# Kernel tuning notes

Measured on AMD Instinct MI355X. Metric: run time of the kernel, lower is better.

## Reference

```python
import jax, jax.numpy as jnp
import numpy as np

N_NODES = 100000
N_EDGES = 600000
HIDDEN = 128


def setup_inputs() -> dict:
    key = jax.random.key(0)
    ks = jax.random.split(key, 5)
    x = jax.random.normal(ks[0], (N_NODES, HIDDEN), dtype=jnp.float32)
    edge_index = jax.random.randint(ks[1], (2, N_EDGES), 0, N_NODES, dtype=jnp.int64)
    edge_weight = jax.random.uniform(ks[2], (N_EDGES,), dtype=jnp.float32)
    # MLP params: Linear(2*H+1 -> H), ReLU, Linear(H -> 1)
    W1 = jax.random.normal(ks[3], (2 * HIDDEN + 1, HIDDEN), dtype=jnp.float32) * (1.0 / np.sqrt(2 * HIDDEN + 1))
    b1 = jnp.zeros((HIDDEN,), dtype=jnp.float32)
    W2 = jax.random.normal(ks[4], (HIDDEN, 1), dtype=jnp.float32) * (1.0 / np.sqrt(HIDDEN))
    b2 = jnp.zeros((1,), dtype=jnp.float32)
    return {"x": x, "edge_index": edge_index, "edge_weight": edge_weight,
            "W1": W1, "b1": b1, "W2": W2, "b2": b2}


def reference(x, edge_index, edge_weight, W1, b1, W2, b2):
    num_nodes = x.shape[0]
    src = edge_index[0]
    tgt = edge_index[1]
    h_src = x[src]                      # [E, H] gather
    h_tgt = x[tgt]                      # [E, H] gather
    w = edge_weight[:, None]            # [E, 1]
    concat = jnp.concatenate([h_src, h_tgt, w], axis=-1)   # [E, 2H+1]
    hidden = jax.nn.relu(concat @ W1 + b1)                 # [E, H]
    scores = (hidden @ W2 + b2)[:, 0]                      # [E]
    # NOTE: the original _softmax_edge's max-pass uses index_put_(accumulate=True)
    # on a -inf buffer, so every touched entry stays -inf and is then replaced by 0;
    # the net effect is NO max subtraction. Faithful math: plain exp / segment_sum.
    exp_scores = jnp.exp(scores)
    sum_exp = jax.ops.segment_sum(exp_scores, tgt, num_segments=num_nodes)
    sum_exp = jnp.maximum(sum_exp, 1e-12)
    alpha = exp_scores / sum_exp[tgt]                      # [E]
    out = jax.ops.segment_sum(alpha[:, None] * h_src, tgt, num_segments=num_nodes)
    return x + out
```

## Files before the change

### kernel.cpp

```cpp
#include <hip/hip_runtime.h>
#include <hip/hip_bf16.h>

#define N_NODES 100000
#define N_EDGES 600000
#define HID 128
#define SCAN_NB ((N_NODES + 255) / 256)


typedef short bf16x8 __attribute__((ext_vector_type(8)));
typedef float f32x4  __attribute__((ext_vector_type(4)));

__device__ inline unsigned short f2bf(float v) {
    __hip_bfloat16 h = __float2bfloat16(v);
    return *(unsigned short*)&h;
}
__device__ inline float bf2f(unsigned short s) {
    unsigned int u = (unsigned int)s << 16;
    return __uint_as_float(u);
}
__device__ inline float2 bfpair(unsigned int u) {
    float lo = __uint_as_float(u << 16);
    float hi = __uint_as_float(u & 0xffff0000u);
    return make_float2(lo, hi);
}

__global__ __launch_bounds__(256) void k_prep(const float* __restrict__ W1,
                                              unsigned short* __restrict__ Bh,
                                              int* __restrict__ deg)
{
    int idx = blockIdx.x * 256 + threadIdx.x;
    if (idx < N_NODES) deg[idx] = 0;
    if (idx < 32768) {
        int n = idx & 255;
        int k = idx >> 8;
        float v = (n < HID) ? W1[k * HID + n] : W1[(HID + k) * HID + (n - HID)];
        int dst = (k >> 5) * 8192 + n * 32 + (k & 31);
        Bh[dst] = f2bf(v);
    }
}

__global__ __launch_bounds__(256) void k_gemm(const float* __restrict__ x,
                                              const unsigned short* __restrict__ BhG,
                                              unsigned short* __restrict__ zbuf,
                                              unsigned short* __restrict__ y2buf)
{
    __shared__ unsigned short Ah[64 * 32];

    const int tid  = threadIdx.x;
    const int bm   = blockIdx.x * 64;
    const int wave = tid >> 6;
    const int lane = tid & 63;
    const int q    = lane >> 4;
    const int ln   = lane & 15;

    const int rowA = tid >> 3;
    const int rowB = rowA + 32;
    const int f4   = tid & 7;
    const int gmA  = bm + rowA;
    const int gmB  = bm + rowB;
    const bool okA = gmA < N_NODES;
    const bool okB = gmB < N_NODES;
    const float* pxA = &x[(size_t)gmA * HID + f4 * 4];
    const float* pxB = &x[(size_t)gmB * HID + f4 * 4];

    f32x4 acc[4][4] = {};

    float4 vA = make_float4(0.f,0.f,0.f,0.f), vB = vA;
    float4 vAn = vA, vBn = vA;
    if (okA) vA = *(const float4*)pxA;
    if (okB) vB = *(const float4*)pxB;

    for (int ks = 0; ks < 4; ++ks) {
        const int k0 = ks * 32;
        {
            float4 v = vA;
            unsigned int ph0 = (unsigned int)f2bf(v.x) | ((unsigned int)f2bf(v.y) << 16);
            unsigned int ph1 = (unsigned int)f2bf(v.z) | ((unsigned int)f2bf(v.w) << 16);
            *(uint2*)&Ah[rowA * 32 + f4 * 4] = make_uint2(ph0, ph1);
            if (okA) *(uint2*)&zbuf[(size_t)gmA * 256 + 128 + k0 + f4 * 4] = make_uint2(ph0, ph1);
        }
        {
            float4 v = vB;
            unsigned int ph0 = (unsigned int)f2bf(v.x) | ((unsigned int)f2bf(v.y) << 16);
            unsigned int ph1 = (unsigned int)f2bf(v.z) | ((unsigned int)f2bf(v.w) << 16);
            *(uint2*)&Ah[rowB * 32 + f4 * 4] = make_uint2(ph0, ph1);
            if (okB) *(uint2*)&zbuf[(size_t)gmB * 256 + 128 + k0 + f4 * 4] = make_uint2(ph0, ph1);
        }
        __syncthreads();

        if (ks < 3) {
            vAn = okA ? *(const float4*)(pxA + (ks + 1) * 32) : make_float4(0.f,0.f,0.f,0.f);
            vBn = okB ? *(const float4*)(pxB + (ks + 1) * 32) : make_float4(0.f,0.f,0.f,0.f);
        }

        bf16x8 ah[4], bh[4];
        #pragma unroll
        for (int mt = 0; mt < 4; ++mt) {
            ah[mt] = *(const bf16x8*)&Ah[(mt * 16 + ln) * 32 + q * 8];
        }
        #pragma unroll
        for (int nt = 0; nt < 4; ++nt) {
            bh[nt] = *(const bf16x8*)&BhG[ks * 8192 + (wave * 64 + nt * 16 + ln) * 32 + q * 8];
        }
        #pragma unroll
        for (int mt = 0; mt < 4; ++mt) {
            #pragma unroll
            for (int nt = 0; nt < 4; ++nt) {
                acc[mt][nt] = __builtin_amdgcn_mfma_f32_16x16x32_bf16(ah[mt], bh[nt], acc[mt][nt], 0, 0, 0);
            }
        }
        __syncthreads();
        vA = vAn; vB = vBn;
    }

    #pragma unroll
    for (int mt = 0; mt < 4; ++mt) {
        #pragma unroll
        for (int r = 0; r < 4; ++r) {
            int row = bm + mt * 16 + q * 4 + r;
            if (row < N_NODES) {
                #pragma unroll
                for (int nt = 0; nt < 4; ++nt) {
                    int col = wave * 64 + nt * 16 + ln;
                    unsigned short v = f2bf(acc[mt][nt][r]);
                    if (col < 128) zbuf[(size_t)row * 256 + col] = v;
                    else           y2buf[(size_t)row * 128 + (col - 128)] = v;
                }
            }
        }
    }
}

__global__ __launch_bounds__(256) void k_count(const int* __restrict__ ei,
                                               int* __restrict__ deg)
{
    int e = blockIdx.x * blockDim.x + threadIdx.x;
    if (e < N_EDGES) atomicAdd(&deg[ei[N_EDGES + e]], 1);
}

__global__ __launch_bounds__(256) void k_partial(const int* __restrict__ deg,
                                                 int* __restrict__ partial)
{
    __shared__ int s[256];
    int t = threadIdx.x;
    int idx = blockIdx.x * 256 + t;
    s[t] = (idx < N_NODES) ? deg[idx] : 0;
    __syncthreads();
    #pragma unroll
    for (int off = 128; off > 0; off >>= 1) {
        if (t < off) s[t] += s[t + off];
        __syncthreads();
    }
    if (t == 0) partial[blockIdx.x] = s[0];
}

__global__ __launch_bounds__(512) void k_scanp(const int* __restrict__ partial,
                                               int* __restrict__ pbase)
{
    __shared__ int s[512];
    int t = threadIdx.x;
    int v = (t < SCAN_NB) ? partial[t] : 0;
    s[t] = v;
    __syncthreads();
    #pragma unroll
    for (int off = 1; off < 512; off <<= 1) {
        int u = (t >= off) ? s[t - off] : 0;
        __syncthreads();
        s[t] += u;
        __syncthreads();
    }
    if (t < SCAN_NB) pbase[t] = s[t] - v;
}

__global__ __launch_bounds__(256) void k_rowptr(const int* __restrict__ deg,
                                                const int* __restrict__ pbase,
                                                int* __restrict__ rowptr,
                                                int* __restrict__ cursor)
{
    __shared__ int s[256];
    int t = threadIdx.x;
    int b = blockIdx.x;
    int idx = b * 256 + t;
    int v = (idx < N_NODES) ? deg[idx] : 0;
    s[t] = v;
    __syncthreads();
    #pragma unroll
    for (int off = 1; off < 256; off <<= 1) {
        int u = (t >= off) ? s[t - off] : 0;
        __syncthreads();
        s[t] += u;
        __syncthreads();
    }
    if (idx < N_NODES) {
        int r = pbase[b] + s[t] - v;
        rowptr[idx] = r;
        cursor[idx] = r;
    }
    if (idx == 0) rowptr[N_NODES] = N_EDGES;
}

__global__ __launch_bounds__(256) void k_fill(const int* __restrict__ ei,
                                              const float* __restrict__ ew,
                                              int* __restrict__ cursor,
                                              uint2* __restrict__ eprs)
{
    int e = blockIdx.x * blockDim.x + threadIdx.x;
    if (e >= N_EDGES) return;
    int tgt = ei[N_EDGES + e];
    int pos = atomicAdd(&cursor[tgt], 1);
    eprs[pos] = make_uint2((unsigned int)ei[e], __float_as_uint(ew[e]));
}

__global__ __launch_bounds__(256) void k_fused(const unsigned int* __restrict__ zu,
                                               const unsigned int* __restrict__ y2u,
                                               const int* __restrict__ rowptr,
                                               const uint2* __restrict__ eprs,
                                               const float* __restrict__ x,
                                               const float* __restrict__ W1,
                                               const float* __restrict__ b1,
                                               const float* __restrict__ W2,
                                               const float* __restrict__ b2,
                                               float* __restrict__ out)
{
    int n = (blockIdx.x * blockDim.x + threadIdx.x) >> 6;
    int lane = threadIdx.x & 63;
    if (n >= N_NODES) return;
    int ql = lane & 15;
    int qi = lane >> 4;
    int c0 = ql * 8;

    uint4 uy2 = *(const uint4*)&y2u[(size_t)n * 64 + ql * 4];
    float2 y2a = bfpair(uy2.x), y2b = bfpair(uy2.y), y2c = bfpair(uy2.z), y2d = bfpair(uy2.w);
    float4 bv0 = *(const float4*)&b1[c0];
    float4 bv1 = *(const float4*)&b1[c0 + 4];
    float4 wr0 = *(const float4*)&W1[256 * HID + c0];
    float4 wr1 = *(const float4*)&W1[256 * HID + c0 + 4];
    float4 w20 = *(const float4*)&W2[c0];
    float4 w21 = *(const float4*)&W2[c0 + 4];
    float p0 = y2a.x + bv0.x, p1 = y2a.y + bv0.y, p2 = y2b.x + bv0.z, p3 = y2b.y + bv0.w;
    float p4 = y2c.x + bv1.x, p5 = y2c.y + bv1.y, p6 = y2d.x + bv1.z, p7 = y2d.y + bv1.w;
    float b2v = b2[0];

    int beg = rowptr[n], end = rowptr[n + 1];
    float a0 = 0.f, a1 = 0.f, a2 = 0.f, a3 = 0.f;
    float a4 = 0.f, a5 = 0.f, a6 = 0.f, a7 = 0.f;
    float denom = 0.f;

    for (int i = beg; i < end; i += 4) {
        int idx = i + qi;
        bool valid = idx < end;
        int ie = valid ? idx : (end - 1);
        uint2 ep = eprs[ie];
        size_t base = (size_t)ep.x * 128;
        float w = __uint_as_float(ep.y);
        uint4 uy = *(const uint4*)&zu[base + ql * 4];
        uint4 ux = *(const uint4*)&zu[base + 64 + ql * 4];

        float2 ya = bfpair(uy.x), yb = bfpair(uy.y), yc = bfpair(uy.z), yd = bfpair(uy.w);
        float h0 = fmaxf(fmaf(w, wr0.x, ya.x + p0), 0.f);
        float h1 = fmaxf(fmaf(w, wr0.y, ya.y + p1), 0.f);
        float h2 = fmaxf(fmaf(w, wr0.z, yb.x + p2), 0.f);
        float h3 = fmaxf(fmaf(w, wr0.w, yb.y + p3), 0.f);
        float h4 = fmaxf(fmaf(w, wr1.x, yc.x + p4), 0.f);
        float h5 = fmaxf(fmaf(w, wr1.y, yc.y + p5), 0.f);
        float h6 = fmaxf(fmaf(w, wr1.z, yd.x + p6), 0.f);
        float h7 = fmaxf(fmaf(w, wr1.w, yd.y + p7), 0.f);
        float s = ((h0 * w20.x + h1 * w20.y) + (h2 * w20.z + h3 * w20.w))
                + ((h4 * w21.x + h5 * w21.y) + (h6 * w21.z + h7 * w21.w));
        #pragma unroll
        for (int m = 1; m <= 8; m <<= 1) s += __shfl_xor(s, m, 64);
        float es = valid ? __expf(s + b2v) : 0.f;

        float2 xa = bfpair(ux.x), xb = bfpair(ux.y), xc = bfpair(ux.z), xd = bfpair(ux.w);
        a0 = fmaf(es, xa.x, a0); a1 = fmaf(es, xa.y, a1);
        a2 = fmaf(es, xb.x, a2); a3 = fmaf(es, xb.y, a3);
        a4 = fmaf(es, xc.x, a4); a5 = fmaf(es, xc.y, a5);
        a6 = fmaf(es, xd.x, a6); a7 = fmaf(es, xd.y, a7);
        denom += es;
    }

    #pragma unroll
    for (int m = 16; m <= 32; m <<= 1) {
        a0 += __shfl_xor(a0, m, 64); a1 += __shfl_xor(a1, m, 64);
        a2 += __shfl_xor(a2, m, 64); a3 += __shfl_xor(a3, m, 64);
        a4 += __shfl_xor(a4, m, 64); a5 += __shfl_xor(a5, m, 64);
        a6 += __shfl_xor(a6, m, 64); a7 += __shfl_xor(a7, m, 64);
        denom += __shfl_xor(denom, m, 64);
    }

    if (qi == 0) {
        float4 xt0 = *(const float4*)&x[(size_t)n * HID + c0];
        float4 xt1 = *(const float4*)&x[(size_t)n * HID + c0 + 4];
        float inv = 1.0f / fmaxf(denom, 1e-12f);
        float4 o0, o1;
        o0.x = xt0.x + a0 * inv; o0.y = xt0.y + a1 * inv;
        o0.z = xt0.z + a2 * inv; o0.w = xt0.w + a3 * inv;
        o1.x = xt1.x + a4 * inv; o1.y = xt1.y + a5 * inv;
        o1.z = xt1.z + a6 * inv; o1.w = xt1.w + a7 * inv;
        *(float4*)&out[(size_t)n * HID + c0]     = o0;
        *(float4*)&out[(size_t)n * HID + c0 + 4] = o1;
    }
}

extern "C" void kernel_launch(void* const* d_in, const int* in_sizes, int n_in,
                              void* d_out, int out_size, void* d_ws, size_t ws_size,
                              hipStream_t stream) {
    const float* x  = (const float*)d_in[0];
    const int*   ei = (const int*)d_in[1];
    const float* ew = (const float*)d_in[2];
    const float* W1 = (const float*)d_in[3];
    const float* b1 = (const float*)d_in[4];
    const float* W2 = (const float*)d_in[5];
    const float* b2 = (const float*)d_in[6];
    float* out = (float*)d_out;
    char* ws = (char*)d_ws;

    const size_t deg_b    = 400000;
    const size_t rowptr_b = 400016;
    const size_t cursor_b = 400000;
    const size_t eprs_b   = 4800000;
    const size_t part_b   = 1568;
    const size_t pb_b     = 1568;
    const size_t Bh_b     = 65536;

    char* p = ws;
    int* deg      = (int*)p;             p += deg_b;
    int* rowptr   = (int*)p;             p += rowptr_b;
    int* cursor   = (int*)p;             p += cursor_b;
    uint2* eprs   = (uint2*)p;           p += eprs_b;
    int* partial  = (int*)p;             p += part_b;
    int* pbase    = (int*)p;             p += pb_b;
    unsigned short* BhG = (unsigned short*)p;  p += Bh_b;
    unsigned short* zbuf  = (unsigned short*)p;  p += (size_t)N_NODES * 256 * 2;
    unsigned short* y2buf = (unsigned short*)p;

    const int edge_blocks = (N_EDGES + 255) / 256;
    const int node_wave_blocks = (N_NODES * 64 + 255) / 256;
    const int gemm_blocks = (N_NODES + 63) / 64;

    hipLaunchKernelGGL(k_prep, dim3(SCAN_NB), dim3(256), 0, stream, W1, BhG, deg);
    hipLaunchKernelGGL(k_count, dim3(edge_blocks), dim3(256), 0, stream, ei, deg);
    hipLaunchKernelGGL(k_partial, dim3(SCAN_NB), dim3(256), 0, stream, deg, partial);
    hipLaunchKernelGGL(k_scanp, dim3(1), dim3(512), 0, stream, partial, pbase);
    hipLaunchKernelGGL(k_rowptr, dim3(SCAN_NB), dim3(256), 0, stream, deg, pbase, rowptr, cursor);
    hipLaunchKernelGGL(k_fill, dim3(edge_blocks), dim3(256), 0, stream, ei, ew, cursor, eprs);
    hipLaunchKernelGGL(k_gemm, dim3(gemm_blocks), dim3(256), 0, stream, x, BhG, zbuf, y2buf);
    hipLaunchKernelGGL(k_fused, dim3(node_wave_blocks), dim3(256), 0, stream,
                       (const unsigned int*)zbuf, (const unsigned int*)y2buf,
                       rowptr, eprs, x, W1, b1, W2, b2, out);
}
```

Baseline: 277.0 us.

## Merge CSR build into cooperative kernel and co-schedule fill with GEMM

```diff
diff --git a/kernel.cpp b/kernel.cpp
--- a/kernel.cpp
+++ b/kernel.cpp
@@ -1,10 +1,15 @@
 #include <hip/hip_runtime.h>
 #include <hip/hip_bf16.h>
+#include <hip/hip_cooperative_groups.h>
+
+namespace cg = cooperative_groups;
 
 #define N_NODES 100000
 #define N_EDGES 600000
 #define HID 128
-#define SCAN_NB ((N_NODES + 255) / 256)
+#define SCAN_NB 391
+#define GEMM_BLOCKS 1563
+#define FILL_BLOCKS 586
 
 
 typedef short bf16x8 __attribute__((ext_vector_type(8)));
@@ -13,10 +18,6 @@
 __device__ inline unsigned short f2bf(float v) {
     __hip_bfloat16 h = __float2bfloat16(v);
     return *(unsigned short*)&h;
-}
-__device__ inline float bf2f(unsigned short s) {
-    unsigned int u = (unsigned int)s << 16;
-    return __uint_as_float(u);
 }
 __device__ inline float2 bfpair(unsigned int u) {
     float lo = __uint_as_float(u << 16);
@@ -24,27 +25,85 @@
     return make_float2(lo, hi);
 }
 
-__global__ __launch_bounds__(256) void k_prep(const float* __restrict__ W1,
-                                              unsigned short* __restrict__ Bh,
-                                              int* __restrict__ deg)
+__global__ __launch_bounds__(256) void k_csr(const float* __restrict__ W1,
+                                             const int* __restrict__ ei,
+                                             unsigned short* __restrict__ Bh,
+                                             int* __restrict__ deg,
+                                             int* __restrict__ partial,
+                                             int* __restrict__ rowptr,
+                                             int* __restrict__ cursor)
 {
-    int idx = blockIdx.x * 256 + threadIdx.x;
-    if (idx < N_NODES) deg[idx] = 0;
-    if (idx < 32768) {
-        int n = idx & 255;
-        int k = idx >> 8;
+    cg::grid_group grid = cg::this_grid();
+    const int tid  = threadIdx.x;
+    const int b    = blockIdx.x;
+    const int gtid = b * 256 + tid;
+
+    if (gtid < N_NODES) deg[gtid] = 0;
+    if (gtid == 0) rowptr[N_NODES] = N_EDGES;
+    if (gtid < 32768) {
+        int n = gtid & 255;
+        int k = gtid >> 8;
         float v = (n < HID) ? W1[k * HID + n] : W1[(HID + k) * HID + (n - HID)];
-        int dst = (k >> 5) * 8192 + n * 32 + (k & 31);
-        Bh[dst] = f2bf(v);
-    }
-}
-
-__global__ __launch_bounds__(256) void k_gemm(const float* __restrict__ x,
-                                              const unsigned short* __restrict__ BhG,
-                                              unsigned short* __restrict__ zbuf,
-                                              unsigned short* __restrict__ y2buf)
+        Bh[(k >> 5) * 8192 + n * 32 + (k & 31)] = f2bf(v);
+    }
+    grid.sync();
+
+    for (int e = gtid; e < N_EDGES; e += SCAN_NB * 256)
+        atomicAdd(&deg[ei[N_EDGES + e]], 1);
+    grid.sync();
+
+    __shared__ int s[256];
+    int v = (gtid < N_NODES) ? deg[gtid] : 0;
+    s[tid] = v;
+    __syncthreads();
+    #pragma unroll
+    for (int off = 1; off < 256; off <<= 1) {
+        int u = (tid >= off) ? s[tid - off] : 0;
+        __syncthreads();
+        s[tid] += u;
+        __syncthreads();
+    }
+    int incl = s[tid];
+    if (tid == 255) partial[b] = incl;
+    grid.sync();
+
+    int acc = 0;
+    for (int i = tid; i < b; i += 256) acc += partial[i];
+    s[tid] = acc;
+    __syncthreads();
+    #pragma unroll
+    for (int off = 128; off > 0; off >>= 1) {
+        if (tid < off) s[tid] += s[tid + off];
+        __syncthreads();
+    }
+    int pb = s[0];
+    if (gtid < N_NODES) {
+        int r = pb + incl - v;
+        rowptr[gtid] = r;
+        cursor[gtid] = r;
+    }
+}
+
+__global__ __launch_bounds__(256) void k_gemm_fill(const float* __restrict__ x,
+                                                   const unsigned short* __restrict__ BhG,
+                                                   unsigned short* __restrict__ zbuf,
+                                                   unsigned short* __restrict__ y2buf,
+                                                   const int* __restrict__ ei,
+                                                   const float* __restrict__ ew,
+                                                   int* __restrict__ cursor,
+                                                   uint2* __restrict__ eprs)
 {
     __shared__ unsigned short Ah[64 * 32];
+
+    if (blockIdx.x >= GEMM_BLOCKS) {
+        int fb = blockIdx.x - GEMM_BLOCKS;
+        for (int e = fb * 256 + threadIdx.x; e < N_EDGES; e += FILL_BLOCKS * 256) {
+            int tgt = ei[N_EDGES + e];
+            int pos = atomicAdd(&cursor[tgt], 1);
+            eprs[pos] = make_uint2((unsigned int)ei[e], __float_as_uint(ew[e]));
+        }
+        return;
+    }
 
     const int tid  = threadIdx.x;
     const int bm   = blockIdx.x * 64;
@@ -106,7 +165,7 @@
         for (int mt = 0; mt < 4; ++mt) {
             #pragma unroll
             for (int nt = 0; nt < 4; ++nt) {
-                acc[mt][nt] = __builtin_amdgcn_mfma_f32_16x16x32_bf16(ah[mt], bh[nt], acc[mt][nt], 0, 0, 0);
+                acc[mt][nt] = __builtin_amdgcn_mfma_f32_16x16x32_bf16(bh[nt], ah[mt], acc[mt][nt], 0, 0, 0);
             }
         }
         __syncthreads();
@@ -115,100 +174,18 @@
 
     #pragma unroll
     for (int mt = 0; mt < 4; ++mt) {
-        #pragma unroll
-        for (int r = 0; r < 4; ++r) {
-            int row = bm + mt * 16 + q * 4 + r;
-            if (row < N_NODES) {
-                #pragma unroll
-                for (int nt = 0; nt < 4; ++nt) {
-                    int col = wave * 64 + nt * 16 + ln;
-                    unsigned short v = f2bf(acc[mt][nt][r]);
-                    if (col < 128) zbuf[(size_t)row * 256 + col] = v;
-                    else           y2buf[(size_t)row * 128 + (col - 128)] = v;
-                }
+        int node = bm + mt * 16 + ln;
+        if (node < N_NODES) {
+            #pragma unroll
+            for (int nt = 0; nt < 4; ++nt) {
+                int col0 = wave * 64 + nt * 16 + q * 4;
+                unsigned int lo = (unsigned int)f2bf(acc[mt][nt][0]) | ((unsigned int)f2bf(acc[mt][nt][1]) << 16);
+                unsigned int hi = (unsigned int)f2bf(acc[mt][nt][2]) | ((unsigned int)f2bf(acc[mt][nt][3]) << 16);
+                if (col0 < 128) *(uint2*)&zbuf[(size_t)node * 256 + col0] = make_uint2(lo, hi);
+                else            *(uint2*)&y2buf[(size_t)node * 128 + (col0 - 128)] = make_uint2(lo, hi);
             }
         }
     }
-}
-
-__global__ __launch_bounds__(256) void k_count(const int* __restrict__ ei,
-                                               int* __restrict__ deg)
-{
-    int e = blockIdx.x * blockDim.x + threadIdx.x;
-    if (e < N_EDGES) atomicAdd(&deg[ei[N_EDGES + e]], 1);
-}
-
-__global__ __launch_bounds__(256) void k_partial(const int* __restrict__ deg,
-                                                 int* __restrict__ partial)
-{
-    __shared__ int s[256];
-    int t = threadIdx.x;
-    int idx = blockIdx.x * 256 + t;
-    s[t] = (idx < N_NODES) ? deg[idx] : 0;
-    __syncthreads();
-    #pragma unroll
-    for (int off = 128; off > 0; off >>= 1) {
-        if (t < off) s[t] += s[t + off];
-        __syncthreads();
-    }
-    if (t == 0) partial[blockIdx.x] = s[0];
-}
-
-__global__ __launch_bounds__(512) void k_scanp(const int* __restrict__ partial,
-                                               int* __restrict__ pbase)
-{
-    __shared__ int s[512];
-    int t = threadIdx.x;
-    int v = (t < SCAN_NB) ? partial[t] : 0;
-    s[t] = v;
-    __syncthreads();
-    #pragma unroll
-    for (int off = 1; off < 512; off <<= 1) {
-        int u = (t >= off) ? s[t - off] : 0;
-        __syncthreads();
-        s[t] += u;
-        __syncthreads();
-    }
-    if (t < SCAN_NB) pbase[t] = s[t] - v;
-}
-
-__global__ __launch_bounds__(256) void k_rowptr(const int* __restrict__ deg,
-                                                const int* __restrict__ pbase,
-                                                int* __restrict__ rowptr,
-                                                int* __restrict__ cursor)
-{
-    __shared__ int s[256];
-    int t = threadIdx.x;
-    int b = blockIdx.x;
-    int idx = b * 256 + t;
-    int v = (idx < N_NODES) ? deg[idx] : 0;
-    s[t] = v;
-    __syncthreads();
-    #pragma unroll
-    for (int off = 1; off < 256; off <<= 1) {
-        int u = (t >= off) ? s[t - off] : 0;
-        __syncthreads();
-        s[t] += u;
-        __syncthreads();
-    }
-    if (idx < N_NODES) {
-        int r = pbase[b] + s[t] - v;
-        rowptr[idx] = r;
-        cursor[idx] = r;
-    }
-    if (idx == 0) rowptr[N_NODES] = N_EDGES;
-}
-
-__global__ __launch_bounds__(256) void k_fill(const int* __restrict__ ei,
-                                              const float* __restrict__ ew,
-                                              int* __restrict__ cursor,
-                                              uint2* __restrict__ eprs)
-{
-    int e = blockIdx.x * blockDim.x + threadIdx.x;
-    if (e >= N_EDGES) return;
-    int tgt = ei[N_EDGES + e];
-    int pos = atomicAdd(&cursor[tgt], 1);
-    eprs[pos] = make_uint2((unsigned int)ei[e], __float_as_uint(ew[e]));
 }
 
 __global__ __launch_bounds__(256) void k_fused(const unsigned int* __restrict__ zu,
@@ -329,22 +306,20 @@
     int* cursor   = (int*)p;             p += cursor_b;
     uint2* eprs   = (uint2*)p;           p += eprs_b;
     int* partial  = (int*)p;             p += part_b;
-    int* pbase    = (int*)p;             p += pb_b;
+    p += pb_b;
     unsigned short* BhG = (unsigned short*)p;  p += Bh_b;
     unsigned short* zbuf  = (unsigned short*)p;  p += (size_t)N_NODES * 256 * 2;
     unsigned short* y2buf = (unsigned short*)p;
 
-    const int edge_blocks = (N_EDGES + 255) / 256;
     const int node_wave_blocks = (N_NODES * 64 + 255) / 256;
-    const int gemm_blocks = (N_NODES + 63) / 64;
-
-    hipLaunchKernelGGL(k_prep, dim3(SCAN_NB), dim3(256), 0, stream, W1, BhG, deg);
-    hipLaunchKernelGGL(k_count, dim3(edge_blocks), dim3(256), 0, stream, ei, deg);
-    hipLaunchKernelGGL(k_partial, dim3(SCAN_NB), dim3(256), 0, stream, deg, partial);
-    hipLaunchKernelGGL(k_scanp, dim3(1), dim3(512), 0, stream, partial, pbase);
-    hipLaunchKernelGGL(k_rowptr, dim3(SCAN_NB), dim3(256), 0, stream, deg, pbase, rowptr, cursor);
-    hipLaunchKernelGGL(k_fill, dim3(edge_blocks), dim3(256), 0, stream, ei, ew, cursor, eprs);
-    hipLaunchKernelGGL(k_gemm, dim3(gemm_blocks), dim3(256), 0, stream, x, BhG, zbuf, y2buf);
+
+    void* csr_args[] = {(void*)&W1, (void*)&ei, (void*)&BhG, (void*)&deg,
+                        (void*)&partial, (void*)&rowptr, (void*)&cursor};
+    hipLaunchCooperativeKernel(k_csr, dim3(SCAN_NB), dim3(256), csr_args, 0u, stream);
+
+    hipLaunchKernelGGL(k_gemm_fill, dim3(GEMM_BLOCKS + FILL_BLOCKS), dim3(256), 0, stream,
+                       x, BhG, zbuf, y2buf, ei, ew, cursor, eprs);
+
     hipLaunchKernelGGL(k_fused, dim3(node_wave_blocks), dim3(256), 0, stream,
                        (const unsigned int*)zbuf, (const unsigned int*)y2buf,
                        rowptr, eprs, x, W1, b1, W2, b2, out);
```

New measurement: 420.2 us. 1.52x slower.

## Merge CSR fill into GEMM launch and fold partial-sum scan into rowptr

Applied to the files above, without the earlier changes.

```diff
diff --git a/kernel.cpp b/kernel.cpp
--- a/kernel.cpp
+++ b/kernel.cpp
@@ -4,7 +4,9 @@
 #define N_NODES 100000
 #define N_EDGES 600000
 #define HID 128
-#define SCAN_NB ((N_NODES + 255) / 256)
+#define SCAN_NB 391
+#define GEMM_BLOCKS 1563
+#define FILL_BLOCKS 586
 
 
 typedef short bf16x8 __attribute__((ext_vector_type(8)));
@@ -13,10 +15,6 @@
 __device__ inline unsigned short f2bf(float v) {
     __hip_bfloat16 h = __float2bfloat16(v);
     return *(unsigned short*)&h;
-}
-__device__ inline float bf2f(unsigned short s) {
-    unsigned int u = (unsigned int)s << 16;
-    return __uint_as_float(u);
 }
 __device__ inline float2 bfpair(unsigned int u) {
     float lo = __uint_as_float(u << 16);
@@ -34,17 +32,93 @@
         int n = idx & 255;
         int k = idx >> 8;
         float v = (n < HID) ? W1[k * HID + n] : W1[(HID + k) * HID + (n - HID)];
-        int dst = (k >> 5) * 8192 + n * 32 + (k & 31);
-        Bh[dst] = f2bf(v);
-    }
-}
-
-__global__ __launch_bounds__(256) void k_gemm(const float* __restrict__ x,
-                                              const unsigned short* __restrict__ BhG,
-                                              unsigned short* __restrict__ zbuf,
-                                              unsigned short* __restrict__ y2buf)
+        Bh[(k >> 5) * 8192 + n * 32 + (k & 31)] = f2bf(v);
+    }
+}
+
+__global__ __launch_bounds__(256) void k_count(const int* __restrict__ ei,
+                                               int* __restrict__ deg)
+{
+    int e = blockIdx.x * blockDim.x + threadIdx.x;
+    if (e < N_EDGES) atomicAdd(&deg[ei[N_EDGES + e]], 1);
+}
+
+__global__ __launch_bounds__(256) void k_partial(const int* __restrict__ deg,
+                                                 int* __restrict__ partial)
+{
+    __shared__ int s[256];
+    int t = threadIdx.x;
+    int idx = blockIdx.x * 256 + t;
+    s[t] = (idx < N_NODES) ? deg[idx] : 0;
+    __syncthreads();
+    #pragma unroll
+    for (int off = 128; off > 0; off >>= 1) {
+        if (t < off) s[t] += s[t + off];
+        __syncthreads();
+    }
+    if (t == 0) partial[blockIdx.x] = s[0];
+}
+
+__global__ __launch_bounds__(256) void k_rowptr(const int* __restrict__ deg,
+                                                const int* __restrict__ partial,
+                                                int* __restrict__ rowptr,
+                                                int* __restrict__ cursor)
+{
+    __shared__ int sp[256];
+    __shared__ int s[256];
+    int t = threadIdx.x;
+    int b = blockIdx.x;
+
+    int acc = 0;
+    for (int i = t; i < b; i += 256) acc += partial[i];
+    sp[t] = acc;
+    __syncthreads();
+    #pragma unroll
+    for (int off = 128; off > 0; off >>= 1) {
+        if (t < off) sp[t] += sp[t + off];
+        __syncthreads();
+    }
+    int pb = sp[0];
+
+    int idx = b * 256 + t;
+    int v = (idx < N_NODES) ? deg[idx] : 0;
+    s[t] = v;
+    __syncthreads();
+    #pragma unroll
+    for (int off = 1; off < 256; off <<= 1) {
+        int u = (t >= off) ? s[t - off] : 0;
+        __syncthreads();
+        s[t] += u;
+        __syncthreads();
+    }
+    if (idx < N_NODES) {
+        int r = pb + s[t] - v;
+        rowptr[idx] = r;
+        cursor[idx] = r;
+    }
+    if (idx == 0) rowptr[N_NODES] = N_EDGES;
+}
+
+__global__ __launch_bounds__(256) void k_gemm_fill(const float* __restrict__ x,
+                                                   const unsigned short* __restrict__ BhG,
+                                                   unsigned short* __restrict__ zbuf,
+                                                   unsigned short* __restrict__ y2buf,
+                                                   const int* __restrict__ ei,
+                                                   const float* __restrict__ ew,
+                                                   int* __restrict__ cursor,
+                                                   uint2* __restrict__ eprs)
 {
     __shared__ unsigned short Ah[64 * 32];
+
+    if (blockIdx.x >= GEMM_BLOCKS) {
+        int fb = blockIdx.x - GEMM_BLOCKS;
+        for (int e = fb * 256 + threadIdx.x; e < N_EDGES; e += FILL_BLOCKS * 256) {
+            int tgt = ei[N_EDGES + e];
+            int pos = atomicAdd(&cursor[tgt], 1);
+            eprs[pos] = make_uint2((unsigned int)ei[e], __float_as_uint(ew[e]));
+        }
+        return;
+    }
 
     const int tid  = threadIdx.x;
     const int bm   = blockIdx.x * 64;
@@ -106,7 +180,7 @@
         for (int mt = 0; mt < 4; ++mt) {
             #pragma unroll
             for (int nt = 0; nt < 4; ++nt) {
-                acc[mt][nt] = __builtin_amdgcn_mfma_f32_16x16x32_bf16(ah[mt], bh[nt], acc[mt][nt], 0, 0, 0);
+                acc[mt][nt] = __builtin_amdgcn_mfma_f32_16x16x32_bf16(bh[nt], ah[mt], acc[mt][nt], 0, 0, 0);
             }
         }
         __syncthreads();
@@ -115,100 +189,18 @@
 
     #pragma unroll
     for (int mt = 0; mt < 4; ++mt) {
-        #pragma unroll
-        for (int r = 0; r < 4; ++r) {
-            int row = bm + mt * 16 + q * 4 + r;
-            if (row < N_NODES) {
-                #pragma unroll
-                for (int nt = 0; nt < 4; ++nt) {
-                    int col = wave * 64 + nt * 16 + ln;
-                    unsigned short v = f2bf(acc[mt][nt][r]);
-                    if (col < 128) zbuf[(size_t)row * 256 + col] = v;
-                    else           y2buf[(size_t)row * 128 + (col - 128)] = v;
-                }
+        int node = bm + mt * 16 + ln;
+        if (node < N_NODES) {
+            #pragma unroll
+            for (int nt = 0; nt < 4; ++nt) {
+                int col0 = wave * 64 + nt * 16 + q * 4;
+                unsigned int lo = (unsigned int)f2bf(acc[mt][nt][0]) | ((unsigned int)f2bf(acc[mt][nt][1]) << 16);
+                unsigned int hi = (unsigned int)f2bf(acc[mt][nt][2]) | ((unsigned int)f2bf(acc[mt][nt][3]) << 16);
+                if (col0 < 128) *(uint2*)&zbuf[(size_t)node * 256 + col0] = make_uint2(lo, hi);
+                else            *(uint2*)&y2buf[(size_t)node * 128 + (col0 - 128)] = make_uint2(lo, hi);
             }
         }
     }
-}
-
-__global__ __launch_bounds__(256) void k_count(const int* __restrict__ ei,
-                                               int* __restrict__ deg)
-{
-    int e = blockIdx.x * blockDim.x + threadIdx.x;
-    if (e < N_EDGES) atomicAdd(&deg[ei[N_EDGES + e]], 1);
-}
-
-__global__ __launch_bounds__(256) void k_partial(const int* __restrict__ deg,
-                                                 int* __restrict__ partial)
-{
-    __shared__ int s[256];
-    int t = threadIdx.x;
-    int idx = blockIdx.x * 256 + t;
-    s[t] = (idx < N_NODES) ? deg[idx] : 0;
-    __syncthreads();
-    #pragma unroll
-    for (int off = 128; off > 0; off >>= 1) {
-        if (t < off) s[t] += s[t + off];
-        __syncthreads();
-    }
-    if (t == 0) partial[blockIdx.x] = s[0];
-}
-
-__global__ __launch_bounds__(512) void k_scanp(const int* __restrict__ partial,
-                                               int* __restrict__ pbase)
-{
-    __shared__ int s[512];
-    int t = threadIdx.x;
-    int v = (t < SCAN_NB) ? partial[t] : 0;
-    s[t] = v;
-    __syncthreads();
-    #pragma unroll
-    for (int off = 1; off < 512; off <<= 1) {
-        int u = (t >= off) ? s[t - off] : 0;
-        __syncthreads();
-        s[t] += u;
-        __syncthreads();
-    }
-    if (t < SCAN_NB) pbase[t] = s[t] - v;
-}
-
-__global__ __launch_bounds__(256) void k_rowptr(const int* __restrict__ deg,
-                                                const int* __restrict__ pbase,
-                                                int* __restrict__ rowptr,
-                                                int* __restrict__ cursor)
-{
-    __shared__ int s[256];
-    int t = threadIdx.x;
-    int b = blockIdx.x;
-    int idx = b * 256 + t;
-    int v = (idx < N_NODES) ? deg[idx] : 0;
-    s[t] = v;
-    __syncthreads();
-    #pragma unroll
-    for (int off = 1; off < 256; off <<= 1) {
-        int u = (t >= off) ? s[t - off] : 0;
-        __syncthreads();
-        s[t] += u;
-        __syncthreads();
-    }
-    if (idx < N_NODES) {
-        int r = pbase[b] + s[t] - v;
-        rowptr[idx] = r;
-        cursor[idx] = r;
-    }
-    if (idx == 0) rowptr[N_NODES] = N_EDGES;
-}
-
-__global__ __launch_bounds__(256) void k_fill(const int* __restrict__ ei,
-                                              const float* __restrict__ ew,
-                                              int* __restrict__ cursor,
-                                              uint2* __restrict__ eprs)
-{
-    int e = blockIdx.x * blockDim.x + threadIdx.x;
-    if (e >= N_EDGES) return;
-    int tgt = ei[N_EDGES + e];
-    int pos = atomicAdd(&cursor[tgt], 1);
-    eprs[pos] = make_uint2((unsigned int)ei[e], __float_as_uint(ew[e]));
 }
 
 __global__ __launch_bounds__(256) void k_fused(const unsigned int* __restrict__ zu,
@@ -329,22 +321,20 @@
     int* cursor   = (int*)p;             p += cursor_b;
     uint2* eprs   = (uint2*)p;           p += eprs_b;
     int* partial  = (int*)p;             p += part_b;
-    int* pbase    = (int*)p;             p += pb_b;
+    p += pb_b;
     unsigned short* BhG = (unsigned short*)p;  p += Bh_b;
     unsigned short* zbuf  = (unsigned short*)p;  p += (size_t)N_NODES * 256 * 2;
     unsigned short* y2buf = (unsigned short*)p;
 
     const int edge_blocks = (N_EDGES + 255) / 256;
     const int node_wave_blocks = (N_NODES * 64 + 255) / 256;
-    const int gemm_blocks = (N_NODES + 63) / 64;
-
-    hipLaunchKernelGGL(k_prep, dim3(SCAN_NB), dim3(256), 0, stream, W1, BhG, deg);
-    hipLaunchKernelGGL(k_count, dim3(edge_blocks), dim3(256), 0, stream, ei, deg);
-    hipLaunchKernelGGL(k_partial, dim3(SCAN_NB), dim3(256), 0, stream, deg, partial);
-    hipLaunchKernelGGL(k_scanp, dim3(1), dim3(512), 0, stream, partial, pbase);
-    hipLaunchKernelGGL(k_rowptr, dim3(SCAN_NB), dim3(256), 0, stream, deg, pbase, rowptr, cursor);
-    hipLaunchKernelGGL(k_fill, dim3(edge_blocks), dim3(256), 0, stream, ei, ew, cursor, eprs);
-    hipLaunchKernelGGL(k_gemm, dim3(gemm_blocks), dim3(256), 0, stream, x, BhG, zbuf, y2buf);
+
+    hipLaunchKernelGGL(k_prep,   dim3(SCAN_NB), dim3(256), 0, stream, W1, BhG, deg);
+    hipLaunchKernelGGL(k_count,  dim3(edge_blocks), dim3(256), 0, stream, ei, deg);
+    hipLaunchKernelGGL(k_partial,dim3(SCAN_NB), dim3(256), 0, stream, deg, partial);
+    hipLaunchKernelGGL(k_rowptr, dim3(SCAN_NB), dim3(256), 0, stream, deg, partial, rowptr, cursor);
+    hipLaunchKernelGGL(k_gemm_fill, dim3(GEMM_BLOCKS + FILL_BLOCKS), dim3(256), 0, stream,
+                       x, BhG, zbuf, y2buf, ei, ew, cursor, eprs);
     hipLaunchKernelGGL(k_fused, dim3(node_wave_blocks), dim3(256), 0, stream,
                        (const unsigned int*)zbuf, (const unsigned int*)y2buf,
                        rowptr, eprs, x, W1, b1, W2, b2, out);
```

Result: faster. 270.0 us (-2.5%).
